# Optimization experiments

Measured on AMD Instinct MI355X. Metric: run time of the kernel, lower is better.

Reference implementation:

```python
import jax, jax.numpy as jnp
import numpy as np

HEAD_DIM = 128
N_HEADS = 32
N_KV = 8
EPS = 1e-6


def setup_inputs() -> dict:
    key = jax.random.key(0)
    ks = jax.random.split(key, 8)
    B, S, H = 1, 2048, 2560
    hidden_states = jax.random.normal(ks[0], (B, S, H), dtype=jnp.float32)
    # rotary embeddings (any values work for a math reference)
    pos = jnp.arange(S, dtype=jnp.float32)[:, None]
    inv_freq = 1.0 / (10000.0 ** (jnp.arange(0, HEAD_DIM, 2, dtype=jnp.float32) / HEAD_DIM))
    ang = pos * inv_freq[None, :]            # [S, HEAD_DIM/2]
    emb = jnp.concatenate([ang, ang], axis=-1)  # [S, HEAD_DIM]
    cos = jnp.cos(emb)[None]                 # [1, S, HEAD_DIM]
    sin = jnp.sin(emb)[None]
    sc = 0.02
    Wq = jax.random.normal(ks[1], (N_HEADS * HEAD_DIM, H), dtype=jnp.float32) * sc
    Wk = jax.random.normal(ks[2], (N_KV * HEAD_DIM, H), dtype=jnp.float32) * sc
    Wv = jax.random.normal(ks[3], (N_KV * HEAD_DIM, H), dtype=jnp.float32) * sc
    Wo = jax.random.normal(ks[4], (H, N_HEADS * HEAD_DIM), dtype=jnp.float32) * sc
    q_norm_w = jnp.ones((HEAD_DIM,), dtype=jnp.float32)
    k_norm_w = jnp.ones((HEAD_DIM,), dtype=jnp.float32)
    return dict(hidden_states=hidden_states, cos=cos, sin=sin,
                Wq=Wq, Wk=Wk, Wv=Wv, Wo=Wo,
                q_norm_w=q_norm_w, k_norm_w=k_norm_w)


def _rms_norm(x, w):
    var = jnp.mean(x * x, axis=-1, keepdims=True)
    return x * jax.lax.rsqrt(var + EPS) * w


def _rotate_half(x):
    x1, x2 = jnp.split(x, 2, axis=-1)
    return jnp.concatenate([-x2, x1], axis=-1)


def reference(hidden_states, cos, sin, Wq, Wk, Wv, Wo, q_norm_w, k_norm_w):
    B, S, H = hidden_states.shape
    scale = HEAD_DIM ** -0.5
    # projections -> [B, heads, S, D]
    q = (hidden_states @ Wq.T).reshape(B, S, N_HEADS, HEAD_DIM)
    k = (hidden_states @ Wk.T).reshape(B, S, N_KV, HEAD_DIM)
    v = (hidden_states @ Wv.T).reshape(B, S, N_KV, HEAD_DIM)
    q = _rms_norm(q, q_norm_w).transpose(0, 2, 1, 3)   # [B, 32, S, D]
    k = _rms_norm(k, k_norm_w).transpose(0, 2, 1, 3)   # [B, 8, S, D]
    v = v.transpose(0, 2, 1, 3)
    # RoPE (cos/sin broadcast over heads via [:, None])
    c = cos[:, None]
    s = sin[:, None]
    q = q * c + _rotate_half(q) * s
    k = k * c + _rotate_half(k) * s
    # GQA: expand kv heads (repeat_kv)
    rep = N_HEADS // N_KV
    k = jnp.repeat(k, rep, axis=1)  # [B, 32, S, D]
    v = jnp.repeat(v, rep, axis=1)
    # causal SDPA (prefill => is_causal=True, full-length cache)
    scores = jnp.einsum('bhqd,bhkd->bhqk', q, k) * scale
    causal = jnp.tril(jnp.ones((S, S), dtype=bool))
    scores = jnp.where(causal, scores, jnp.finfo(scores.dtype).min)
    probs = jax.nn.softmax(scores, axis=-1)
    out = jnp.einsum('bhqk,bhkd->bhqd', probs, v)      # [B, 32, S, D]
    out = out.transpose(0, 2, 1, 3).reshape(B, S, N_HEADS * HEAD_DIM)
    return out @ Wo.T
```

## Files before the change

kernel.cpp:

```cpp
#include <hip/hip_runtime.h>

#define S_LEN   2048
#define HID     2560
#define NH      32
#define NKV     8
#define HD      128
#define QDIM    (NH*HD)
#define KVDIM   (NKV*HD)

typedef __attribute__((ext_vector_type(8))) short short8;
typedef __attribute__((ext_vector_type(4))) float f32x4;

__device__ __forceinline__ unsigned short f2bf(float f) {
    unsigned u = __float_as_uint(f);
    u += 0x7fffu + ((u >> 16) & 1u);
    return (unsigned short)(u >> 16);
}
__device__ __forceinline__ float bf2f(unsigned short s) {
    return __uint_as_float(((unsigned)s) << 16);
}
__device__ __forceinline__ void gload16(const void* g, void* l) {
    __builtin_amdgcn_global_load_lds(
        (const __attribute__((address_space(1))) unsigned int*)g,
        (__attribute__((address_space(3))) unsigned int*)l, 16, 0, 0);
}

#define N4_HS  (S_LEN*HID/4)
#define N4_WQ  (QDIM*HID/4)
#define N4_WKV (KVDIM*HID/4)
__global__ __launch_bounds__(256) void cvt4(
    const float* __restrict__ hs, const float* __restrict__ Wq,
    const float* __restrict__ Wk, const float* __restrict__ Wv,
    unsigned short* __restrict__ hsB, unsigned short* __restrict__ WqB,
    unsigned short* __restrict__ WkB, unsigned short* __restrict__ WvB)
{
    int i = blockIdx.x * 256 + threadIdx.x;
    const float* s; unsigned short* d;
    if (i < N4_HS)                          { s = hs; d = hsB; }
    else if (i < N4_HS + N4_WQ)             { i -= N4_HS; s = Wq; d = WqB; }
    else if (i < N4_HS + N4_WQ + N4_WKV)    { i -= N4_HS + N4_WQ; s = Wk; d = WkB; }
    else                                    { i -= N4_HS + N4_WQ + N4_WKV; s = Wv; d = WvB; }
    float4 v = ((const float4*)s)[i];
    ushort4 o;
    o.x = f2bf(v.x); o.y = f2bf(v.y); o.z = f2bf(v.z); o.w = f2bf(v.w);
    ((ushort4*)d)[i] = o;
}

__global__ __launch_bounds__(256) void cvt_f32_bf16(
    const float* __restrict__ s, unsigned short* __restrict__ d, int n4)
{
    int i = blockIdx.x * 256 + threadIdx.x;
    if (i >= n4) return;
    float4 v = ((const float4*)s)[i];
    ushort4 o;
    o.x = f2bf(v.x); o.y = f2bf(v.y); o.z = f2bf(v.z); o.w = f2bf(v.w);
    ((ushort4*)d)[i] = o;
}

struct GemmRegs {
    f32x4 acc[4][4];
};
__device__ __forceinline__ void gemm_core(
    const unsigned short* A, const unsigned short* B, int Kd,
    unsigned short* As, unsigned short* Bs, GemmRegs& R,
    int rowA0, int rowB0, int tid)
{
    const int lane = tid & 63;
    const int l15 = lane & 15, l4 = lane >> 4;
    const int w = tid >> 6;
    const int wr = (w >> 1) * 64, wc = (w & 1) * 64;
    const int sw = l15 & 7;

#pragma unroll
    for (int i = 0; i < 4; i++)
#pragma unroll
        for (int j = 0; j < 4; j++)
            R.acc[i][j] = (f32x4){0.f, 0.f, 0.f, 0.f};

    for (int k0 = 0; k0 < Kd; k0 += 64) {
        __syncthreads();
#pragma unroll
        for (int i = 0; i < 4; i++) {
            int tc = tid + i * 256;
            int r = tc >> 3, cl = tc & 7;
            int cg = cl ^ (r & 7);
            gload16(A + (size_t)(rowA0 + r) * Kd + k0 + cg * 8, &As[tc * 8]);
            gload16(B + (size_t)(rowB0 + r) * Kd + k0 + cg * 8, &Bs[tc * 8]);
        }
        __syncthreads();

#pragma unroll
        for (int ks = 0; ks < 2; ks++) {
            const int kc = (ks * 4 + l4) ^ sw;
            short8 af[4], bf[4];
#pragma unroll
            for (int i = 0; i < 4; i++)
                af[i] = *(const short8*)&As[(wr + i*16 + l15)*64 + kc*8];
#pragma unroll
            for (int j = 0; j < 4; j++)
                bf[j] = *(const short8*)&Bs[(wc + j*16 + l15)*64 + kc*8];
#pragma unroll
            for (int i = 0; i < 4; i++)
#pragma unroll
                for (int j = 0; j < 4; j++)
                    R.acc[i][j] = __builtin_amdgcn_mfma_f32_16x16x32_bf16(
                        af[i], bf[j], R.acc[i][j], 0, 0, 0);
        }
    }
}

__global__ __launch_bounds__(256) void gemm_bf16(
    const unsigned short* __restrict__ A, const unsigned short* __restrict__ B,
    float* __restrict__ Cf, unsigned short* __restrict__ Cb, int N, int Kd)
{
    __shared__ unsigned short As[128*64];
    __shared__ unsigned short Bs[128*64];
    const int tid = threadIdx.x;
    const int lane = tid & 63, w = tid >> 6;
    const int l15 = lane & 15, l4 = lane >> 4;
    const int wr = (w >> 1) * 64, wc = (w & 1) * 64;
    GemmRegs R;
    gemm_core(A, B, Kd, As, Bs, R, blockIdx.y * 128, blockIdx.x * 128, tid);

#pragma unroll
    for (int i = 0; i < 4; i++)
#pragma unroll
        for (int j = 0; j < 4; j++) {
            int row0 = blockIdx.y*128 + wr + i*16 + l4*4;
            int col  = blockIdx.x*128 + wc + j*16 + l15;
#pragma unroll
            for (int r = 0; r < 4; r++) {
                size_t off = (size_t)(row0 + r) * N + col;
                if (Cf) Cf[off] = R.acc[i][j][r];
                else    Cb[off] = f2bf(R.acc[i][j][r]);
            }
        }
}

__global__ __launch_bounds__(256) void gemm_qkv(
    const unsigned short* __restrict__ A,
    const unsigned short* __restrict__ Wq, const unsigned short* __restrict__ Wk,
    const unsigned short* __restrict__ Wv,
    unsigned short* __restrict__ Qo, unsigned short* __restrict__ Ko,
    unsigned short* __restrict__ Vo)
{
    __shared__ unsigned short As[128*64];
    __shared__ unsigned short Bs[128*64];
    const int bx = blockIdx.x;
    const unsigned short* B;
    unsigned short* C;
    int ldc, cb;
    if (bx < 32)      { B = Wq + (size_t)bx*128*HID;      C = Qo; ldc = QDIM;  cb = bx*128; }
    else if (bx < 40) { B = Wk + (size_t)(bx-32)*128*HID; C = Ko; ldc = KVDIM; cb = (bx-32)*128; }
    else              { B = Wv + (size_t)(bx-40)*128*HID; C = Vo; ldc = KVDIM; cb = (bx-40)*128; }

    const int tid = threadIdx.x;
    const int lane = tid & 63, w = tid >> 6;
    const int l15 = lane & 15, l4 = lane >> 4;
    const int wr = (w >> 1) * 64, wc = (w & 1) * 64;
    GemmRegs R;
    gemm_core(A, B, HID, As, Bs, R, blockIdx.y * 128, 0, tid);

#pragma unroll
    for (int i = 0; i < 4; i++)
#pragma unroll
        for (int j = 0; j < 4; j++) {
            int row0 = blockIdx.y*128 + wr + i*16 + l4*4;
            int col  = cb + wc + j*16 + l15;
#pragma unroll
            for (int r = 0; r < 4; r++)
                C[(size_t)(row0 + r) * ldc + col] = f2bf(R.acc[i][j][r]);
        }
}

__global__ __launch_bounds__(256) void rmsnorm_rope_bf16(
    unsigned short* __restrict__ X, const float* __restrict__ w,
    const float* __restrict__ ct, const float* __restrict__ st, int nheads)
{
    int wid  = (blockIdx.x * blockDim.x + threadIdx.x) >> 6;
    int lane = threadIdx.x & 63;
    int s = wid / nheads;
    int h = wid - s * nheads;
    unsigned short* x = X + (size_t)s * (nheads * HD) + h * HD;

    float x1 = bf2f(x[lane]);
    float x2 = bf2f(x[lane + 64]);
    float ss = x1*x1 + x2*x2;
#pragma unroll
    for (int off = 32; off > 0; off >>= 1) ss += __shfl_xor(ss, off, 64);
    float r = rsqrtf(ss * (1.0f/128.0f) + 1e-6f);
    float n1 = x1 * r * w[lane];
    float n2 = x2 * r * w[lane + 64];
    float c1 = ct[s*HD + lane],      s1 = st[s*HD + lane];
    float c2 = ct[s*HD + lane + 64], s2 = st[s*HD + lane + 64];
    x[lane]      = f2bf(n1*c1 - n2*s1);
    x[lane + 64] = f2bf(n2*c2 + n1*s2);
}

__global__ __launch_bounds__(256, 3) void flash_mfma(
    const unsigned short* __restrict__ Q, const unsigned short* __restrict__ K,
    const unsigned short* __restrict__ V, unsigned short* __restrict__ O)
{
    const int pb = blockIdx.x;
    const int h = blockIdx.y, kvh = h >> 2;
    const int tid = threadIdx.x;
    const int w = tid >> 6, lane = tid & 63;
    const int l15 = lane & 15, l4 = lane >> 4;

    __shared__ unsigned short Ks[64*128];
    __shared__ unsigned short Vt[128*72];
    __shared__ unsigned short Ps[4*16*72];
    __shared__ float Lw[4][16];

    const float scale2 = 0.08838834764831845f * 1.4426950408889634f;
    const float M2 = 17.3f;
    unsigned short* Pw = &Ps[w * 16 * 72];

#pragma unroll 1
    for (int phase = 0; phase < 2; phase++) {
        const int qt = phase ? pb : (31 - pb);
        const int q0 = qt * 64;

        short8 qa[4];
        {
            const unsigned short* qg = Q + (size_t)(q0 + w*16 + l15) * QDIM + h * HD;
#pragma unroll
            for (int ka = 0; ka < 4; ka++)
                qa[ka] = *(const short8*)(qg + ka*32 + l4*8);
        }

        const f32x4 zero = {0.f, 0.f, 0.f, 0.f};
        f32x4 accO[8];
#pragma unroll
        for (int j = 0; j < 8; j++) accO[j] = zero;
        float lsum = 0.f;

        for (int t = 0; t <= qt; t++) {
            const int c0 = t * 64;
            __syncthreads();
            {
#pragma unroll
                for (int i = 0; i < 4; i++) {
                    int tc = tid + i * 256;
                    int r = tc >> 4, cl = tc & 15;
                    int cg = cl ^ (r & 7);
                    gload16(K + (size_t)(c0 + r) * KVDIM + kvh * HD + cg * 8,
                            &Ks[tc * 8]);
                }
            }
            {
                int rp = tid & 15, cgv = tid >> 4;
                const unsigned short* vg = V + (size_t)(c0 + 4*rp) * KVDIM + kvh * HD + cgv * 8;
                union { int4 v; unsigned short s[8]; } u0, u1, u2, u3;
                u0.v = *(const int4*)vg;
                u1.v = *(const int4*)(vg + KVDIM);
                u2.v = *(const int4*)(vg + 2*KVDIM);
                u3.v = *(const int4*)(vg + 3*KVDIM);
#pragma unroll
                for (int i = 0; i < 8; i++) {
                    uint2 pk;
                    pk.x = (unsigned)u0.s[i] | ((unsigned)u1.s[i] << 16);
                    pk.y = (unsigned)u2.s[i] | ((unsigned)u3.s[i] << 16);
                    *(uint2*)&Vt[(cgv*8 + i)*72 + 4*rp] = pk;
                }
            }
            __syncthreads();

            f32x4 sc[4];
#pragma unroll
            for (int mt = 0; mt < 4; mt++) sc[mt] = zero;
#pragma unroll
            for (int ka = 0; ka < 4; ka++) {
#pragma unroll
                for (int mt = 0; mt < 4; mt++) {
                    int row = mt*16 + l15;
                    int cs = (ka*4 + l4) ^ (row & 7);
                    short8 kb = *(const short8*)&Ks[row*128 + cs*8];
                    sc[mt] = __builtin_amdgcn_mfma_f32_16x16x32_bf16(kb, qa[ka], sc[mt], 0, 0, 0);
                }
            }

            const int qglob = q0 + w*16 + l15;
            const bool diag = (t == qt);
#pragma unroll
            for (int mt = 0; mt < 4; mt++) {
                float pv[4];
#pragma unroll
                for (int r = 0; r < 4; r++) {
                    int kvg = c0 + mt*16 + l4*4 + r;
                    float e = __builtin_amdgcn_exp2f(fmaf(sc[mt][r], scale2, -M2));
                    pv[r] = (!diag || kvg <= qglob) ? e : 0.f;
                    lsum += pv[r];
                }
                uint2 pk;
                pk.x = (unsigned)f2bf(pv[0]) | ((unsigned)f2bf(pv[1]) << 16);
                pk.y = (unsigned)f2bf(pv[2]) | ((unsigned)f2bf(pv[3]) << 16);
                *(uint2*)&Pw[l15*72 + mt*16 + l4*4] = pk;
            }

#pragma unroll
            for (int ks = 0; ks < 2; ks++) {
                short8 pf = *(const short8*)&Pw[l15*72 + ks*32 + l4*8];
#pragma unroll
                for (int dt = 0; dt < 8; dt++) {
                    short8 vf = *(const short8*)&Vt[(dt*16 + l15)*72 + ks*32 + l4*8];
                    accO[dt] = __builtin_amdgcn_mfma_f32_16x16x32_bf16(pf, vf, accO[dt], 0, 0, 0);
                }
            }
        }

        lsum += __shfl_xor(lsum, 16, 64);
        lsum += __shfl_xor(lsum, 32, 64);
        if (l4 == 0) Lw[w][l15] = lsum;
        f32x4 linv;
#pragma unroll
        for (int r = 0; r < 4; r++) linv[r] = 1.0f / Lw[w][l4*4 + r];

#pragma unroll
        for (int dt = 0; dt < 8; dt++)
#pragma unroll
            for (int r = 0; r < 4; r++) {
                int row_l = w*16 + l4*4 + r;
                O[(size_t)(q0 + row_l) * QDIM + h*HD + dt*16 + l15] =
                    f2bf(accO[dt][r] * linv[r]);
            }
    }
}

extern "C" void kernel_launch(void* const* d_in, const int* in_sizes, int n_in,
                              void* d_out, int out_size, void* d_ws, size_t ws_size,
                              hipStream_t stream)
{
    const float* hs   = (const float*)d_in[0];
    const float* cosb = (const float*)d_in[1];
    const float* sinb = (const float*)d_in[2];
    const float* Wq   = (const float*)d_in[3];
    const float* Wk   = (const float*)d_in[4];
    const float* Wv   = (const float*)d_in[5];
    const float* Wo   = (const float*)d_in[6];
    const float* qw   = (const float*)d_in[7];
    const float* kw   = (const float*)d_in[8];
    float* out = (float*)d_out;

    char* ws = (char*)d_ws;
    unsigned short* hsB = (unsigned short*)(ws);
    unsigned short* WqB = (unsigned short*)(ws + 10485760);
    unsigned short* WkB = (unsigned short*)(ws + 31457280);
    unsigned short* WvB = (unsigned short*)(ws + 36700160);
    unsigned short* KB  = (unsigned short*)(ws + 41943040);
    unsigned short* VB  = (unsigned short*)(ws + 46137344);
    unsigned short* WoB = (unsigned short*)(ws + 41943040);
    unsigned short* QB  = (unsigned short*)(ws + 62914560);
    unsigned short* CB  = (unsigned short*)(ws + 18874368);

    {
        int n4 = N4_HS + N4_WQ + 2 * N4_WKV;
        cvt4<<<(n4+255)/256, 256, 0, stream>>>(hs, Wq, Wk, Wv, hsB, WqB, WkB, WvB);
    }

    gemm_qkv<<<dim3(48, S_LEN/128), 256, 0, stream>>>(hsB, WqB, WkB, WvB, QB, KB, VB);

    rmsnorm_rope_bf16<<<S_LEN*NH/4,  256, 0, stream>>>(QB, qw, cosb, sinb, NH);
    rmsnorm_rope_bf16<<<S_LEN*NKV/4, 256, 0, stream>>>(KB, kw, cosb, sinb, NKV);

    flash_mfma<<<dim3(16, NH), 256, 0, stream>>>(QB, KB, VB, CB);

    cvt_f32_bf16<<<(HID*QDIM/4+255)/256, 256, 0, stream>>>(Wo, WoB, HID*QDIM/4);

    gemm_bf16<<<dim3(HID/128, S_LEN/128), 256, 0, stream>>>(CB, WoB, out, nullptr, HID, QDIM);
}
```

Baseline: 405.1 us.

## Write V transposed from QKV GEMM and async-load it in flash attention

The QKV GEMM now writes V in a per-kv-head transposed layout [kvh][d][s], so the attention kernel can bring V tiles into swizzled LDS with async global-to-LDS loads. This replaces the register-based transpose done on every tile. The flash kernel also drops the two-phase balanced pairing of query tiles and launches one block per query tile (32x32 grid), ordered longest-first. Float-to-bf16 conversions use the packed HIP intrinsic. The risks are scattered transposed stores in the GEMM epilogue and a more uneven per-block workload.

```diff
diff --git a/kernel.cpp b/kernel.cpp
--- a/kernel.cpp
+++ b/kernel.cpp
@@ -1,4 +1,5 @@
 #include <hip/hip_runtime.h>
+#include <hip/hip_bf16.h>
 
 #define S_LEN   2048
 #define HID     2560
@@ -18,6 +19,10 @@
 }
 __device__ __forceinline__ float bf2f(unsigned short s) {
     return __uint_as_float(((unsigned)s) << 16);
+}
+__device__ __forceinline__ unsigned pk2bf(float a, float b) {
+    __hip_bfloat162 h = __float22bfloat162_rn(make_float2(a, b));
+    union { __hip_bfloat162 h; unsigned u; } c; c.h = h; return c.u;
 }
 __device__ __forceinline__ void gload16(const void* g, void* l) {
     __builtin_amdgcn_global_load_lds(
@@ -41,9 +46,9 @@
     else if (i < N4_HS + N4_WQ + N4_WKV)    { i -= N4_HS + N4_WQ; s = Wk; d = WkB; }
     else                                    { i -= N4_HS + N4_WQ + N4_WKV; s = Wv; d = WvB; }
     float4 v = ((const float4*)s)[i];
-    ushort4 o;
-    o.x = f2bf(v.x); o.y = f2bf(v.y); o.z = f2bf(v.z); o.w = f2bf(v.w);
-    ((ushort4*)d)[i] = o;
+    uint2 o;
+    o.x = pk2bf(v.x, v.y); o.y = pk2bf(v.z, v.w);
+    ((uint2*)d)[i] = o;
 }
 
 __global__ __launch_bounds__(256) void cvt_f32_bf16(
@@ -52,9 +57,9 @@
     int i = blockIdx.x * 256 + threadIdx.x;
     if (i >= n4) return;
     float4 v = ((const float4*)s)[i];
-    ushort4 o;
-    o.x = f2bf(v.x); o.y = f2bf(v.y); o.z = f2bf(v.z); o.w = f2bf(v.w);
-    ((ushort4*)d)[i] = o;
+    uint2 o;
+    o.x = pk2bf(v.x, v.y); o.y = pk2bf(v.z, v.w);
+    ((uint2*)d)[i] = o;
 }
 
 struct GemmRegs {
@@ -142,17 +147,15 @@
     const unsigned short* __restrict__ Wq, const unsigned short* __restrict__ Wk,
     const unsigned short* __restrict__ Wv,
     unsigned short* __restrict__ Qo, unsigned short* __restrict__ Ko,
-    unsigned short* __restrict__ Vo)
+    unsigned short* __restrict__ VTo)
 {
     __shared__ unsigned short As[128*64];
     __shared__ unsigned short Bs[128*64];
     const int bx = blockIdx.x;
     const unsigned short* B;
-    unsigned short* C;
-    int ldc, cb;
-    if (bx < 32)      { B = Wq + (size_t)bx*128*HID;      C = Qo; ldc = QDIM;  cb = bx*128; }
-    else if (bx < 40) { B = Wk + (size_t)(bx-32)*128*HID; C = Ko; ldc = KVDIM; cb = (bx-32)*128; }
-    else              { B = Wv + (size_t)(bx-40)*128*HID; C = Vo; ldc = KVDIM; cb = (bx-40)*128; }
+    if (bx < 32)      B = Wq + (size_t)bx*128*HID;
+    else if (bx < 40) B = Wk + (size_t)(bx-32)*128*HID;
+    else              B = Wv + (size_t)(bx-40)*128*HID;
 
     const int tid = threadIdx.x;
     const int lane = tid & 63, w = tid >> 6;
@@ -161,16 +164,36 @@
     GemmRegs R;
     gemm_core(A, B, HID, As, Bs, R, blockIdx.y * 128, 0, tid);
 
-#pragma unroll
-    for (int i = 0; i < 4; i++)
-#pragma unroll
-        for (int j = 0; j < 4; j++) {
-            int row0 = blockIdx.y*128 + wr + i*16 + l4*4;
-            int col  = cb + wc + j*16 + l15;
-#pragma unroll
-            for (int r = 0; r < 4; r++)
-                C[(size_t)(row0 + r) * ldc + col] = f2bf(R.acc[i][j][r]);
-        }
+    if (bx < 40) {
+        unsigned short* C; int ldc, cb;
+        if (bx < 32) { C = Qo; ldc = QDIM;  cb = bx*128; }
+        else         { C = Ko; ldc = KVDIM; cb = (bx-32)*128; }
+#pragma unroll
+        for (int i = 0; i < 4; i++)
+#pragma unroll
+            for (int j = 0; j < 4; j++) {
+                int row0 = blockIdx.y*128 + wr + i*16 + l4*4;
+                int col  = cb + wc + j*16 + l15;
+#pragma unroll
+                for (int r = 0; r < 4; r++)
+                    C[(size_t)(row0 + r) * ldc + col] = f2bf(R.acc[i][j][r]);
+            }
+    } else {
+        const int cbase = (bx - 40) * 128;
+#pragma unroll
+        for (int i = 0; i < 4; i++)
+#pragma unroll
+            for (int j = 0; j < 4; j++) {
+                int col  = cbase + wc + j*16 + l15;
+                int row0 = blockIdx.y*128 + wr + i*16 + l4*4;
+                int kvhh = col >> 7, d = col & 127;
+                unsigned short* p = VTo + (size_t)kvhh*HD*S_LEN + (size_t)d*S_LEN + row0;
+                uint2 pk;
+                pk.x = pk2bf(R.acc[i][j][0], R.acc[i][j][1]);
+                pk.y = pk2bf(R.acc[i][j][2], R.acc[i][j][3]);
+                *(uint2*)p = pk;
+            }
+    }
 }
 
 __global__ __launch_bounds__(256) void rmsnorm_rope_bf16(
@@ -199,132 +222,122 @@
 
 __global__ __launch_bounds__(256, 3) void flash_mfma(
     const unsigned short* __restrict__ Q, const unsigned short* __restrict__ K,
-    const unsigned short* __restrict__ V, unsigned short* __restrict__ O)
-{
-    const int pb = blockIdx.x;
+    const unsigned short* __restrict__ VT, unsigned short* __restrict__ O)
+{
+    const int qt = 31 - (int)blockIdx.x;
     const int h = blockIdx.y, kvh = h >> 2;
     const int tid = threadIdx.x;
     const int w = tid >> 6, lane = tid & 63;
     const int l15 = lane & 15, l4 = lane >> 4;
+    const int q0 = qt * 64;
 
     __shared__ unsigned short Ks[64*128];
-    __shared__ unsigned short Vt[128*72];
+    __shared__ unsigned short Vt[128*64];
     __shared__ unsigned short Ps[4*16*72];
     __shared__ float Lw[4][16];
 
     const float scale2 = 0.08838834764831845f * 1.4426950408889634f;
     const float M2 = 17.3f;
     unsigned short* Pw = &Ps[w * 16 * 72];
-
-#pragma unroll 1
-    for (int phase = 0; phase < 2; phase++) {
-        const int qt = phase ? pb : (31 - pb);
-        const int q0 = qt * 64;
-
-        short8 qa[4];
+    const unsigned short* VTh = VT + (size_t)kvh * HD * S_LEN;
+
+    short8 qa[4];
+    {
+        const unsigned short* qg = Q + (size_t)(q0 + w*16 + l15) * QDIM + h * HD;
+#pragma unroll
+        for (int ka = 0; ka < 4; ka++)
+            qa[ka] = *(const short8*)(qg + ka*32 + l4*8);
+    }
+
+    const f32x4 zero = {0.f, 0.f, 0.f, 0.f};
+    f32x4 accO[8];
+#pragma unroll
+    for (int j = 0; j < 8; j++) accO[j] = zero;
+    float lsum = 0.f;
+
+    for (int t = 0; t <= qt; t++) {
+        const int c0 = t * 64;
+        __syncthreads();
         {
-            const unsigned short* qg = Q + (size_t)(q0 + w*16 + l15) * QDIM + h * HD;
-#pragma unroll
-            for (int ka = 0; ka < 4; ka++)
-                qa[ka] = *(const short8*)(qg + ka*32 + l4*8);
-        }
-
-        const f32x4 zero = {0.f, 0.f, 0.f, 0.f};
-        f32x4 accO[8];
-#pragma unroll
-        for (int j = 0; j < 8; j++) accO[j] = zero;
-        float lsum = 0.f;
-
-        for (int t = 0; t <= qt; t++) {
-            const int c0 = t * 64;
-            __syncthreads();
-            {
-#pragma unroll
-                for (int i = 0; i < 4; i++) {
-                    int tc = tid + i * 256;
-                    int r = tc >> 4, cl = tc & 15;
-                    int cg = cl ^ (r & 7);
-                    gload16(K + (size_t)(c0 + r) * KVDIM + kvh * HD + cg * 8,
-                            &Ks[tc * 8]);
-                }
-            }
-            {
-                int rp = tid & 15, cgv = tid >> 4;
-                const unsigned short* vg = V + (size_t)(c0 + 4*rp) * KVDIM + kvh * HD + cgv * 8;
-                union { int4 v; unsigned short s[8]; } u0, u1, u2, u3;
-                u0.v = *(const int4*)vg;
-                u1.v = *(const int4*)(vg + KVDIM);
-                u2.v = *(const int4*)(vg + 2*KVDIM);
-                u3.v = *(const int4*)(vg + 3*KVDIM);
-#pragma unroll
-                for (int i = 0; i < 8; i++) {
-                    uint2 pk;
-                    pk.x = (unsigned)u0.s[i] | ((unsigned)u1.s[i] << 16);
-                    pk.y = (unsigned)u2.s[i] | ((unsigned)u3.s[i] << 16);
-                    *(uint2*)&Vt[(cgv*8 + i)*72 + 4*rp] = pk;
-                }
-            }
-            __syncthreads();
-
-            f32x4 sc[4];
-#pragma unroll
-            for (int mt = 0; mt < 4; mt++) sc[mt] = zero;
-#pragma unroll
-            for (int ka = 0; ka < 4; ka++) {
-#pragma unroll
-                for (int mt = 0; mt < 4; mt++) {
-                    int row = mt*16 + l15;
-                    int cs = (ka*4 + l4) ^ (row & 7);
-                    short8 kb = *(const short8*)&Ks[row*128 + cs*8];
-                    sc[mt] = __builtin_amdgcn_mfma_f32_16x16x32_bf16(kb, qa[ka], sc[mt], 0, 0, 0);
-                }
-            }
-
-            const int qglob = q0 + w*16 + l15;
-            const bool diag = (t == qt);
+#pragma unroll
+            for (int i = 0; i < 4; i++) {
+                int tc = tid + i * 256;
+                int r = tc >> 4, cl = tc & 15;
+                int cg = cl ^ (r & 7);
+                gload16(K + (size_t)(c0 + r) * KVDIM + kvh * HD + cg * 8,
+                        &Ks[tc * 8]);
+            }
+        }
+        {
+#pragma unroll
+            for (int i = 0; i < 4; i++) {
+                int tc = tid + i * 256;
+                int r = tc >> 3, cl = tc & 7;
+                int cg = cl ^ (r & 7);
+                gload16(VTh + (size_t)r * S_LEN + c0 + cg * 8, &Vt[tc * 8]);
+            }
+        }
+        __syncthreads();
+
+        f32x4 sc[4];
+#pragma unroll
+        for (int mt = 0; mt < 4; mt++) sc[mt] = zero;
+#pragma unroll
+        for (int ka = 0; ka < 4; ka++) {
 #pragma unroll
             for (int mt = 0; mt < 4; mt++) {
-                float pv[4];
-#pragma unroll
-                for (int r = 0; r < 4; r++) {
-                    int kvg = c0 + mt*16 + l4*4 + r;
-                    float e = __builtin_amdgcn_exp2f(fmaf(sc[mt][r], scale2, -M2));
-                    pv[r] = (!diag || kvg <= qglob) ? e : 0.f;
-                    lsum += pv[r];
-                }
-                uint2 pk;
-                pk.x = (unsigned)f2bf(pv[0]) | ((unsigned)f2bf(pv[1]) << 16);
-                pk.y = (unsigned)f2bf(pv[2]) | ((unsigned)f2bf(pv[3]) << 16);
-                *(uint2*)&Pw[l15*72 + mt*16 + l4*4] = pk;
-            }
-
-#pragma unroll
-            for (int ks = 0; ks < 2; ks++) {
-                short8 pf = *(const short8*)&Pw[l15*72 + ks*32 + l4*8];
-#pragma unroll
-                for (int dt = 0; dt < 8; dt++) {
-                    short8 vf = *(const short8*)&Vt[(dt*16 + l15)*72 + ks*32 + l4*8];
-                    accO[dt] = __builtin_amdgcn_mfma_f32_16x16x32_bf16(pf, vf, accO[dt], 0, 0, 0);
-                }
-            }
-        }
-
-        lsum += __shfl_xor(lsum, 16, 64);
-        lsum += __shfl_xor(lsum, 32, 64);
-        if (l4 == 0) Lw[w][l15] = lsum;
-        f32x4 linv;
-#pragma unroll
-        for (int r = 0; r < 4; r++) linv[r] = 1.0f / Lw[w][l4*4 + r];
-
-#pragma unroll
-        for (int dt = 0; dt < 8; dt++)
+                int row = mt*16 + l15;
+                int cs = (ka*4 + l4) ^ (row & 7);
+                short8 kb = *(const short8*)&Ks[row*128 + cs*8];
+                sc[mt] = __builtin_amdgcn_mfma_f32_16x16x32_bf16(kb, qa[ka], sc[mt], 0, 0, 0);
+            }
+        }
+
+        const int qglob = q0 + w*16 + l15;
+        const bool diag = (t == qt);
+#pragma unroll
+        for (int mt = 0; mt < 4; mt++) {
+            float pv[4];
 #pragma unroll
             for (int r = 0; r < 4; r++) {
-                int row_l = w*16 + l4*4 + r;
-                O[(size_t)(q0 + row_l) * QDIM + h*HD + dt*16 + l15] =
-                    f2bf(accO[dt][r] * linv[r]);
-            }
-    }
+                int kvg = c0 + mt*16 + l4*4 + r;
+                float e = __builtin_amdgcn_exp2f(fmaf(sc[mt][r], scale2, -M2));
+                pv[r] = (!diag || kvg <= qglob) ? e : 0.f;
+                lsum += pv[r];
+            }
+            uint2 pk;
+            pk.x = pk2bf(pv[0], pv[1]);
+            pk.y = pk2bf(pv[2], pv[3]);
+            *(uint2*)&Pw[l15*72 + mt*16 + l4*4] = pk;
+        }
+
+#pragma unroll
+        for (int ks = 0; ks < 2; ks++) {
+            short8 pf = *(const short8*)&Pw[l15*72 + ks*32 + l4*8];
+            const int cs = (ks*4 + l4) ^ (l15 & 7);
+#pragma unroll
+            for (int dt = 0; dt < 8; dt++) {
+                short8 vf = *(const short8*)&Vt[(dt*16 + l15)*64 + cs*8];
+                accO[dt] = __builtin_amdgcn_mfma_f32_16x16x32_bf16(pf, vf, accO[dt], 0, 0, 0);
+            }
+        }
+    }
+
+    lsum += __shfl_xor(lsum, 16, 64);
+    lsum += __shfl_xor(lsum, 32, 64);
+    if (l4 == 0) Lw[w][l15] = lsum;
+    f32x4 linv;
+#pragma unroll
+    for (int r = 0; r < 4; r++) linv[r] = 1.0f / Lw[w][l4*4 + r];
+
+#pragma unroll
+    for (int dt = 0; dt < 8; dt++)
+#pragma unroll
+        for (int r = 0; r < 4; r++) {
+            int row_l = w*16 + l4*4 + r;
+            O[(size_t)(q0 + row_l) * QDIM + h*HD + dt*16 + l15] =
+                f2bf(accO[dt][r] * linv[r]);
+        }
 }
 
 extern "C" void kernel_launch(void* const* d_in, const int* in_sizes, int n_in,
@@ -348,7 +361,7 @@
     unsigned short* WkB = (unsigned short*)(ws + 31457280);
     unsigned short* WvB = (unsigned short*)(ws + 36700160);
     unsigned short* KB  = (unsigned short*)(ws + 41943040);
-    unsigned short* VB  = (unsigned short*)(ws + 46137344);
+    unsigned short* VT  = (unsigned short*)(ws + 46137344);
     unsigned short* WoB = (unsigned short*)(ws + 41943040);
     unsigned short* QB  = (unsigned short*)(ws + 62914560);
     unsigned short* CB  = (unsigned short*)(ws + 18874368);
@@ -358,12 +371,12 @@
         cvt4<<<(n4+255)/256, 256, 0, stream>>>(hs, Wq, Wk, Wv, hsB, WqB, WkB, WvB);
     }
 
-    gemm_qkv<<<dim3(48, S_LEN/128), 256, 0, stream>>>(hsB, WqB, WkB, WvB, QB, KB, VB);
+    gemm_qkv<<<dim3(48, S_LEN/128), 256, 0, stream>>>(hsB, WqB, WkB, WvB, QB, KB, VT);
 
     rmsnorm_rope_bf16<<<S_LEN*NH/4,  256, 0, stream>>>(QB, qw, cosb, sinb, NH);
     rmsnorm_rope_bf16<<<S_LEN*NKV/4, 256, 0, stream>>>(KB, kw, cosb, sinb, NKV);
 
-    flash_mfma<<<dim3(16, NH), 256, 0, stream>>>(QB, KB, VB, CB);
+    flash_mfma<<<dim3(32, NH), 256, 0, stream>>>(QB, KB, VT, CB);
 
     cvt_f32_bf16<<<(HID*QDIM/4+255)/256, 256, 0, stream>>>(Wo, WoB, HID*QDIM/4);
 
```

New measurement: 427.2 us. 5.4% more time.
